# Performance work log

Hardware: AMD Instinct MI355X
Metric: run time of the kernel (lower is better)

The kernel has to match this reference:

```python
import jax, jax.numpy as jnp
import numpy as np

B, Z, OUT, NODES = 2048, 64, 512, 64
TRIPLES = 3 * (NODES - 1)  # (self, left, right) per real node
EPS_BN = 1e-5
EPS_TLN = 1e-5
SLOPE = 0.01  # LeakyReLU default


def setup_inputs() -> dict:
    key = jax.random.key(0)
    ks = jax.random.split(key, 12)
    def n(k, shape, s=0.05):
        return jax.random.normal(k, shape, jnp.float32) * s
    inp = {
        "trees": jax.random.normal(ks[0], (B, Z), jnp.float32),
        "indexes": jax.random.randint(ks[1], (B, TRIPLES, 1), 0, NODES),
        # MLP: Linear(Z,64) -> BN -> Linear(64,256) -> BN -> Linear(256,1024) -> BN -> Linear(1024,4096) -> BN
        "w1": n(ks[2], (64, Z)),      "b1": jnp.zeros((64,), jnp.float32),
        "g1": jnp.ones((64,), jnp.float32),   "be1": jnp.zeros((64,), jnp.float32),
        "w2": n(ks[3], (256, 64)),    "b2": jnp.zeros((256,), jnp.float32),
        "g2": jnp.ones((256,), jnp.float32),  "be2": jnp.zeros((256,), jnp.float32),
        "w3": n(ks[4], (1024, 256)),  "b3": jnp.zeros((1024,), jnp.float32),
        "g3": jnp.ones((1024,), jnp.float32), "be3": jnp.zeros((1024,), jnp.float32),
        "w4": n(ks[5], (4096, 1024)), "b4": jnp.zeros((4096,), jnp.float32),
        "g4": jnp.ones((4096,), jnp.float32), "be4": jnp.zeros((4096,), jnp.float32),
        # BinaryTreeConv weights: Conv1d(in,out,kernel=3,stride=3) -> (out,in,3)
        "cw1": n(ks[6], (128, 64, 3)),  "cb1": jnp.zeros((128,), jnp.float32),
        "cw2": n(ks[7], (256, 128, 3)), "cb2": jnp.zeros((256,), jnp.float32),
        "cw3": n(ks[8], (OUT, 256, 3)), "cb3": jnp.zeros((OUT,), jnp.float32),
    }
    return inp


def _bn(x, g, b):
    # BatchNorm1d in training mode: batch statistics, biased variance
    m = jnp.mean(x, axis=0)
    v = jnp.var(x, axis=0)
    return g * (x - m) * jax.lax.rsqrt(v + EPS_BN) + b


def _lrelu(x):
    return jnp.where(x > 0, x, SLOPE * x)


def _tree_conv(x, idx, w, b):
    # x: (B, C, N); idx: (B, 3M) node indices; w: (O, C, 3)
    Bn, C, _ = x.shape
    expanded = jnp.take_along_axis(x, idx[:, None, :], axis=2)  # (B, C, 3M) gather
    expanded = expanded.reshape(Bn, C, -1, 3)                    # (B, C, M, 3)
    out = jnp.einsum('bcmk,ock->bom', expanded, w) + b[None, :, None]
    zero = jnp.zeros((Bn, w.shape[0], 1), x.dtype)               # re-attach null-node slot
    return jnp.concatenate([zero, out], axis=2)                  # (B, O, M+1)


def _tree_norm(x):
    # TreeLayerNorm: normalize over (channels, nodes) per sample; torch.std is unbiased
    m = jnp.mean(x, axis=(1, 2), keepdims=True)
    s = jnp.std(x, axis=(1, 2), ddof=1, keepdims=True)
    return (x - m) / (s + EPS_TLN)


def reference(trees, indexes, w1, b1, g1, be1, w2, b2, g2, be2, w3, b3, g3, be3,
              w4, b4, g4, be4, cw1, cb1, cw2, cb2, cw3, cb3):
    idx = indexes[..., 0]  # (B, 3M)
    h = _lrelu(_bn(trees @ w1.T + b1, g1, be1))
    h = _lrelu(_bn(h @ w2.T + b2, g2, be2))
    h = _lrelu(_bn(h @ w3.T + b3, g3, be3))
    h = _lrelu(_bn(h @ w4.T + b4, g4, be4))
    x = h.reshape(h.shape[0], 64, 64)  # (B, C=64, N=64)
    x = _lrelu(_tree_norm(_tree_conv(x, idx, cw1, cb1)))
    x = _lrelu(_tree_norm(_tree_conv(x, idx, cw2, cb2)))
    x = _lrelu(_tree_norm(_tree_conv(x, idx, cw3, cb3)))
    return x  # (B, OUT, 64)
```

## Files before the change

kernel.cpp:

```cpp
#include <hip/hip_runtime.h>

typedef unsigned short u16;
typedef unsigned int   u32;
typedef __attribute__((ext_vector_type(8))) short short8;
typedef __attribute__((ext_vector_type(4))) float f32x4;
typedef __attribute__((ext_vector_type(4))) u16  u16x4;

#define DI __device__ __forceinline__

DI float b2f(u16 v){ return __builtin_bit_cast(float, (u32)v << 16); }
DI u16 f2b(float f){ u32 u = __builtin_bit_cast(u32, f); return (u16)((u + 0x7fffu + ((u >> 16) & 1u)) >> 16); }
DI float lrelu(float v){ return v > 0.f ? v : 0.01f * v; }

__global__ __launch_bounds__(256)
void cvt_w_all(const float* __restrict__ w1, u16* __restrict__ d1,
               const float* __restrict__ w2, u16* __restrict__ d2,
               const float* __restrict__ w3, u16* __restrict__ d3,
               const float* __restrict__ w4, u16* __restrict__ d4)
{
  int i = blockIdx.x*256 + threadIdx.x;
  const float* s; u16* d; int li;
  if      (i < 1024)   { s = w1; d = d1; li = i; }
  else if (i < 5120)   { s = w2; d = d2; li = i - 1024; }
  else if (i < 70656)  { s = w3; d = d3; li = i - 5120; }
  else if (i < 1119232){ s = w4; d = d4; li = i - 70656; }
  else return;
  float4 v = ((const float4*)s)[li];
  u16x4 o; o[0]=f2b(v.x); o[1]=f2b(v.y); o[2]=f2b(v.z); o[3]=f2b(v.w);
  *(u16x4*)(d + (size_t)li*4) = o;
}

DI void repack_one(const float* __restrict__ w, u16* __restrict__ wr,
                   int e, int C, int lgC)
{
  int R = 3*C;
  int NK   = R >> 5;
  int j    = e & 7;
  int lane = (e >> 3) & 63;
  int blk  = e >> 9;
  int tr   = blk / NK, kb = blk - tr*NK;
  int row  = tr*16 + (lane & 15);
  int kcol = kb*32 + (lane >> 4)*8 + j;
  int k = kcol >> lgC; int c = kcol & (C-1);
  wr[e] = f2b(w[(size_t)row*R + c*3 + k]);
}

__global__ __launch_bounds__(256)
void repack_all(const float* __restrict__ c1, u16* __restrict__ r1,
                const float* __restrict__ c2, u16* __restrict__ r2,
                const float* __restrict__ c3, u16* __restrict__ r3)
{
  int i = blockIdx.x*256 + threadIdx.x;
  if      (i < 24576)  repack_one(c1, r1, i,          64, 6);
  else if (i < 122880) repack_one(c2, r2, i - 24576, 128, 7);
  else if (i < 516096) repack_one(c3, r3, i - 122880,256, 8);
}

template<int BM, int BN, int WROWS, int WCOLS, int RT, int CT, bool APPLY>
__global__ __launch_bounds__(WROWS*WCOLS*64)
void gemm_bn(const float* __restrict__ A, const u16* __restrict__ W,
             const float* __restrict__ partIn, const float* __restrict__ gA,
             const float* __restrict__ beA, int splitIn,
             float* __restrict__ Y, float* __restrict__ partOut,
             int M, int N, int K)
{
  constexpr int NT  = WROWS*WCOLS*64;
  constexpr int ALD = (BM*4)/NT;
  constexpr int BLD = (BN*4)/NT;
  __shared__ __align__(16) u16 As[BM*32];
  __shared__ __align__(16) u16 Bs[BN*32];
  __shared__ float colS[WROWS][BN], colS2[WROWS][BN];
  __shared__ __align__(16) float ssL[APPLY ? 2048 : 4];
  const int tid  = threadIdx.x;
  const int wave = tid >> 6, lane = tid & 63;
  const int wr = wave / WCOLS, wc = wave % WCOLS;
  const int lrow = lane & 15, kg = lane >> 4;
  const int m0 = blockIdx.x * BM, n0 = blockIdx.y * BN;

  if constexpr (APPLY){
    for (int n = tid; n < K; n += NT){
      float s = 0.f, s2 = 0.f;
      for (int i = 0; i < splitIn; i++){
        s  += partIn[(size_t)(i*2+0)*K + n];
        s2 += partIn[(size_t)(i*2+1)*K + n];
      }
      float inv  = 1.f / (float)M;
      float mean = s * inv;
      float var  = fmaxf(s2*inv - mean*mean, 0.f);
      float sc   = gA[n] * rsqrtf(var + 1e-5f);
      ssL[n]     = sc;
      ssL[K + n] = beA[n] - mean*sc;
    }
    __syncthreads();
  }

  f32x4 acc[RT][CT] = {};
  for (int k0 = 0; k0 < K; k0 += 32) {
    uint4 av[ALD], bv[BLD];
#pragma unroll
    for (int i = 0; i < ALD; i++){
      int x = tid + i*NT; int kc = k0 + (x&3)*8;
      const float* ap = A + (size_t)(m0 + (x>>2))*K + kc;
      float4 y0 = *(const float4*)ap, y1 = *(const float4*)(ap + 4);
      float v[8] = {y0.x,y0.y,y0.z,y0.w,y1.x,y1.y,y1.z,y1.w};
      if constexpr (APPLY){
        float4 c0 = *(const float4*)(ssL + kc),     c1 = *(const float4*)(ssL + kc + 4);
        float4 h0 = *(const float4*)(ssL + K + kc), h1 = *(const float4*)(ssL + K + kc + 4);
        v[0]=lrelu(v[0]*c0.x+h0.x); v[1]=lrelu(v[1]*c0.y+h0.y);
        v[2]=lrelu(v[2]*c0.z+h0.z); v[3]=lrelu(v[3]*c0.w+h0.w);
        v[4]=lrelu(v[4]*c1.x+h1.x); v[5]=lrelu(v[5]*c1.y+h1.y);
        v[6]=lrelu(v[6]*c1.z+h1.z); v[7]=lrelu(v[7]*c1.w+h1.w);
      }
      u32 w0 = (u32)f2b(v[0]) | ((u32)f2b(v[1])<<16);
      u32 w1 = (u32)f2b(v[2]) | ((u32)f2b(v[3])<<16);
      u32 w2 = (u32)f2b(v[4]) | ((u32)f2b(v[5])<<16);
      u32 w3 = (u32)f2b(v[6]) | ((u32)f2b(v[7])<<16);
      av[i] = (uint4){w0,w1,w2,w3};
    }
#pragma unroll
    for (int i = 0; i < BLD; i++){ int x = tid + i*NT; bv[i] = *(const uint4*)(W + (size_t)(n0 + (x>>2))*K + k0 + (x&3)*8); }
    __syncthreads();
#pragma unroll
    for (int i = 0; i < ALD; i++){ *(uint4*)(As + (tid + i*NT)*8) = av[i]; }
#pragma unroll
    for (int i = 0; i < BLD; i++){ *(uint4*)(Bs + (tid + i*NT)*8) = bv[i]; }
    __syncthreads();
    short8 af[RT], bfr[CT];
#pragma unroll
    for (int r = 0; r < RT; r++) af[r]  = *(const short8*)(As + ((wr*RT + r)*16 + lrow)*32 + kg*8);
#pragma unroll
    for (int c = 0; c < CT; c++) bfr[c] = *(const short8*)(Bs + ((wc*CT + c)*16 + lrow)*32 + kg*8);
#pragma unroll
    for (int r = 0; r < RT; r++)
#pragma unroll
      for (int c = 0; c < CT; c++)
        acc[r][c] = __builtin_amdgcn_mfma_f32_16x16x32_bf16(af[r], bfr[c], acc[r][c], 0, 0, 0);
  }
#pragma unroll
  for (int r = 0; r < RT; r++)
#pragma unroll
    for (int c = 0; c < CT; c++)
#pragma unroll
      for (int i = 0; i < 4; i++){
        int m = m0 + (wr*RT + r)*16 + kg*4 + i;
        int n = n0 + (wc*CT + c)*16 + lrow;
        Y[(size_t)m*N + n] = acc[r][c][i];
      }
#pragma unroll
  for (int c = 0; c < CT; c++){
    float s = 0.f, s2 = 0.f;
#pragma unroll
    for (int r = 0; r < RT; r++)
#pragma unroll
      for (int i = 0; i < 4; i++){ float v = acc[r][c][i]; s += v; s2 += v*v; }
    s  += __shfl_xor(s, 16);  s  += __shfl_xor(s, 32);
    s2 += __shfl_xor(s2, 16); s2 += __shfl_xor(s2, 32);
    if (kg == 0){ colS[wr][(wc*CT + c)*16 + lrow] = s; colS2[wr][(wc*CT + c)*16 + lrow] = s2; }
  }
  __syncthreads();
  if (tid < BN){
    float S = 0.f, S2 = 0.f;
#pragma unroll
    for (int w = 0; w < WROWS; w++){ S += colS[w][tid]; S2 += colS2[w][tid]; }
    partOut[(size_t)(blockIdx.x*2+0)*N + n0 + tid] = S;
    partOut[(size_t)(blockIdx.x*2+1)*N + n0 + tid] = S2;
  }
}

__global__ __launch_bounds__(256)
void bn_finalize(const float* __restrict__ part, const float* __restrict__ g,
                 const float* __restrict__ be, float* __restrict__ ss, int N, int M, int split)
{
  int n = blockIdx.x*256 + threadIdx.x;
  if (n >= N) return;
  float s = 0.f, s2 = 0.f;
  for (int i = 0; i < split; i++){ s += part[(size_t)(i*2+0)*N + n]; s2 += part[(size_t)(i*2+1)*N + n]; }
  float inv  = 1.f / (float)M;
  float mean = s * inv;
  float var  = fmaxf(s2*inv - mean*mean, 0.f);
  float sc   = g[n] * rsqrtf(var + 1e-5f);
  ss[n]     = sc;
  ss[N + n] = be[n] - mean*sc;
}

template<int C, int O, int WAVES, int MINW, bool PIPE, bool LAST, bool FIRST>
__global__ __launch_bounds__(WAVES*64, MINW)
void conv_norm(const u16* __restrict__ Xin, const float* __restrict__ XinF,
               const float* __restrict__ ssA,
               const u16* __restrict__ Wr,
               const float* __restrict__ cb, const int* __restrict__ gidx,
               u16* __restrict__ Xout, float* __restrict__ Outf)
{
  constexpr int R    = 3*C;
  constexpr int NK   = R/32;
  constexpr int CSI  = C + 8;
  constexpr int RT   = O/(WAVES*16);
  constexpr int NT   = WAVES*64;
  constexpr int LGC  = (C==64)?6:((C==128)?7:8);
  constexpr int LG32 = LGC - 5;
  __shared__ __align__(16) u16 xs[65*CSI];
  __shared__ int idxs[192];
  __shared__ float red[2*WAVES];
  const int b = blockIdx.x, tid = threadIdx.x;
  const int wave = tid >> 6, lane = tid & 63;
  const int lrow = lane & 15, kg = lane >> 4;

  if constexpr (FIRST){
    const float* yg = XinF + (size_t)b*4096;
    int j0 = tid*8;
    float4 a0 = *(const float4*)(yg + j0);
    float4 a1 = *(const float4*)(yg + j0 + 4);
    float4 s0 = *(const float4*)(ssA + j0);
    float4 s1 = *(const float4*)(ssA + j0 + 4);
    float4 h0 = *(const float4*)(ssA + 4096 + j0);
    float4 h1 = *(const float4*)(ssA + 4096 + j0 + 4);
    int c = j0 >> 6, n0 = j0 & 63;
    u16* xp = xs + c;
    xp[(n0+0)*CSI] = f2b(lrelu(a0.x*s0.x + h0.x));
    xp[(n0+1)*CSI] = f2b(lrelu(a0.y*s0.y + h0.y));
    xp[(n0+2)*CSI] = f2b(lrelu(a0.z*s0.z + h0.z));
    xp[(n0+3)*CSI] = f2b(lrelu(a0.w*s0.w + h0.w));
    xp[(n0+4)*CSI] = f2b(lrelu(a1.x*s1.x + h1.x));
    xp[(n0+5)*CSI] = f2b(lrelu(a1.y*s1.y + h1.y));
    xp[(n0+6)*CSI] = f2b(lrelu(a1.z*s1.z + h1.z));
    xp[(n0+7)*CSI] = f2b(lrelu(a1.w*s1.w + h1.w));
  } else {
    const u16* xg = Xin + (size_t)b*64*C;
    for (int e = tid; e < 64*(C/8); e += NT){
      int row = e/(C/8), t = e%(C/8);
      *(uint4*)(xs + row*CSI + t*8) = *(const uint4*)(xg + row*C + t*8);
    }
  }
  for (int e = tid; e < C/8; e += NT){ uint4 z = {0,0,0,0}; *(uint4*)(xs + 64*CSI + e*8) = z; }
  if (tid < 189){ int v = gidx[b*189 + tid]; idxs[tid] = v & 63; }
  __syncthreads();

  int jr0[4], jr1[4], jr2[4];
#pragma unroll
  for (int ct = 0; ct < 4; ct++){
    int n = ct*16 + lrow;
    jr0[ct] = (n == 0) ? 64 : idxs[3*(n-1) + 0];
    jr1[ct] = (n == 0) ? 64 : idxs[3*(n-1) + 1];
    jr2[ct] = (n == 0) ? 64 : idxs[3*(n-1) + 2];
  }

  const u16* wbase = Wr + ((size_t)wave*NK << 9) + lane*8;

  auto loadA = [&](short8* af, int kb32){
#pragma unroll
    for (int r = 0; r < RT; r++)
      af[r] = *(const short8*)(wbase + (((size_t)(WAVES*r)*NK + kb32) << 9));
  };
  auto loadB = [&](short8* bfr, int kb32){
    const int k  = kb32 >> LG32;
    const int c0 = ((kb32*32) & (C-1)) + kg*8;
#pragma unroll
    for (int ct = 0; ct < 4; ct++){
      int row = (k == 0) ? jr0[ct] : ((k == 1) ? jr1[ct] : jr2[ct]);
      bfr[ct] = *(const short8*)(xs + row*CSI + c0);
    }
  };

  f32x4 acc[RT][4] = {};
  auto domfma = [&](short8* af, short8* bfr){
    __builtin_amdgcn_s_setprio(1);
#pragma unroll
    for (int r = 0; r < RT; r++)
#pragma unroll
      for (int ct = 0; ct < 4; ct++)
        acc[r][ct] = __builtin_amdgcn_mfma_f32_16x16x32_bf16(af[r], bfr[ct], acc[r][ct], 0, 0, 0);
    __builtin_amdgcn_s_setprio(0);
  };

  if constexpr (PIPE) {
    short8 afA[RT], bfA[4], afB[RT], bfB[4];
    loadA(afA, 0); loadB(bfA, 0);
    for (int kb32 = 0; kb32 < NK; kb32 += 2){
      loadA(afB, kb32+1); loadB(bfB, kb32+1);
      domfma(afA, bfA);
      if (kb32 + 2 < NK){ loadA(afA, kb32+2); loadB(bfA, kb32+2); }
      domfma(afB, bfB);
    }
  } else {
    for (int kb32 = 0; kb32 < NK; kb32++){
      short8 af[RT], bfr[4];
      loadA(af, kb32); loadB(bfr, kb32);
      domfma(af, bfr);
    }
  }

  float s = 0.f, s2 = 0.f;
#pragma unroll
  for (int r = 0; r < RT; r++)
#pragma unroll
    for (int i = 0; i < 4; i++){
      int o = (wave + WAVES*r)*16 + kg*4 + i;
      float bias = cb[o];
#pragma unroll
      for (int ct = 0; ct < 4; ct++){
        int n = ct*16 + lrow;
        float v = acc[r][ct][i];
        if (n != 0) v += bias;
        acc[r][ct][i] = v;
        s += v; s2 += v*v;
      }
    }
#pragma unroll
  for (int off = 32; off > 0; off >>= 1){ s += __shfl_down(s, off); s2 += __shfl_down(s2, off); }
  if (lane == 0){ red[wave] = s; red[WAVES + wave] = s2; }
  __syncthreads();
  if (tid == 0){
    float S = 0.f, S2 = 0.f;
    for (int w = 0; w < WAVES; w++){ S += red[w]; S2 += red[WAVES + w]; }
    const float NV = (float)(O*64);
    float mean = S / NV;
    float var  = fmaxf(S2/NV - mean*mean, 0.f) * (NV/(NV-1.f));
    float sc   = 1.f / (sqrtf(var) + 1e-5f);
    red[0] = mean; red[1] = sc;
  }
  __syncthreads();
  const float mean = red[0], sc = red[1];

  if constexpr (LAST) {
#pragma unroll
    for (int r = 0; r < RT; r++)
#pragma unroll
      for (int ct = 0; ct < 4; ct++)
#pragma unroll
        for (int i = 0; i < 4; i++){
          int o = (wave + WAVES*r)*16 + kg*4 + i;
          int n = ct*16 + lrow;
          Outf[(size_t)b*(O*64) + o*64 + n] = lrelu((acc[r][ct][i] - mean)*sc);
        }
  } else {
#pragma unroll
    for (int r = 0; r < RT; r++)
#pragma unroll
      for (int ct = 0; ct < 4; ct++){
        int o0 = (wave + WAVES*r)*16 + kg*4;
        int n  = ct*16 + lrow;
        u16x4 pk;
#pragma unroll
        for (int i = 0; i < 4; i++) pk[i] = f2b(lrelu((acc[r][ct][i] - mean)*sc));
        *(u16x4*)(Xout + (size_t)b*64*O + (size_t)n*O + o0) = pk;
      }
  }
}

extern "C" void kernel_launch(void* const* d_in, const int* in_sizes, int n_in,
                              void* d_out, int out_size, void* d_ws, size_t ws_size,
                              hipStream_t stream)
{
  const float* trees = (const float*)d_in[0];
  const int*   gidx  = (const int*)d_in[1];
  const float* w1 = (const float*)d_in[2];
  const float* g1 = (const float*)d_in[4];  const float* be1 = (const float*)d_in[5];
  const float* w2 = (const float*)d_in[6];
  const float* g2 = (const float*)d_in[8];  const float* be2 = (const float*)d_in[9];
  const float* w3 = (const float*)d_in[10];
  const float* g3 = (const float*)d_in[12]; const float* be3 = (const float*)d_in[13];
  const float* w4 = (const float*)d_in[14];
  const float* g4 = (const float*)d_in[16]; const float* be4 = (const float*)d_in[17];
  const float* cw1 = (const float*)d_in[18]; const float* cb1 = (const float*)d_in[19];
  const float* cw2 = (const float*)d_in[20]; const float* cb2 = (const float*)d_in[21];
  const float* cw3 = (const float*)d_in[22]; const float* cb3 = (const float*)d_in[23];

  char* ws = (char*)d_ws;
  size_t off = 0;
  auto alloc = [&](size_t bytes)->char*{ char* p = ws + off; off += (bytes + 255) & ~(size_t)255; return p; };
  u16*   Wr1   = (u16*)  alloc(128*192*2);
  u16*   Wr2   = (u16*)  alloc(256*384*2);
  u16*   Wr3   = (u16*)  alloc(512*768*2);
  float* partA = (float*)alloc(64*4096*4);
  float* partB = (float*)alloc(64*4096*4);
  float* ss4   = (float*)alloc(2*4096*4);
  u16*   Xc3   = (u16*)  alloc((size_t)2048*64*256*2);

  u16*   ob   = (u16*)d_out;
  float* outF = (float*)d_out;
  float* Ya   = (float*)ob;
  u16*   Wb1  = ob + 19660800;
  u16*   Wb2  = ob + 19664896;
  u16*   Wb3  = ob + 19681280;
  u16*   Wb4  = ob + 19943424;
  u16*   Xc2  = ob + 33554432;
  float* Yb   = (float*)(ob + 50331648);

  cvt_w_all <<<4372, 256, 0, stream>>>(w1, Wb1, w2, Wb2, w3, Wb3, w4, Wb4);
  repack_all<<<2016, 256, 0, stream>>>(cw1, Wr1, cw2, Wr2, cw3, Wr3);

  gemm_bn<64,64,4,1,1,4,false><<<dim3(32,1),  256, 0, stream>>>(trees, Wb1, nullptr, nullptr, nullptr, 0,  Ya, partA, 2048, 64,   64);
  gemm_bn<64,64,4,1,1,4,true ><<<dim3(32,4),  256, 0, stream>>>(Ya,    Wb2, partA,   g1,      be1,     32, Yb, partB, 2048, 256,  64);
  gemm_bn<64,64,4,1,1,4,true ><<<dim3(32,16), 256, 0, stream>>>(Yb,    Wb3, partB,   g2,      be2,     32, Ya, partA, 2048, 1024, 256);
  gemm_bn<128,128,2,2,4,4,true><<<dim3(16,32),256, 0, stream>>>(Ya,    Wb4, partA,   g3,      be3,     32, Yb, partB, 2048, 4096, 1024);
  bn_finalize<<<16, 256, 0, stream>>>(partB, g4, be4, ss4, 4096, 2048, 16);

  conv_norm< 64,128,8,4,true ,false,true ><<<2048, 512, 0, stream>>>(nullptr, Yb, ss4, Wr1, cb1, gidx, Xc2, nullptr);
  conv_norm<128,256,8,4,true ,false,false><<<2048, 512, 0, stream>>>(Xc2, nullptr, nullptr, Wr2, cb2, gidx, Xc3, nullptr);
  conv_norm<256,512,8,4,false,true ,false><<<2048, 512, 0, stream>>>(Xc3, nullptr, nullptr, Wr3, cb3, gidx, nullptr, outF);
}
```

Measured before the change: 350.0 us.

## Split conv waves over output and node tiles, half-split A loads in last layer

The tree-conv kernel used to give every wave all 64 node columns and a slice of output channels. It now uses a 2D wave grid (OG output groups × NG node groups), so each wave loads more weight rows and fewer gathered activation tiles. This changes the balance between global weight reads and LDS gather reads per MFMA. The non-pipelined last layer also loads A fragments in two halves, interleaving loads with MFMAs to lower register pressure.

```diff
diff --git a/kernel.cpp b/kernel.cpp
--- a/kernel.cpp
+++ b/kernel.cpp
@@ -183,8 +183,8 @@
   ss[N + n] = be[n] - mean*sc;
 }
 
-template<int C, int O, int WAVES, int MINW, bool PIPE, bool LAST, bool FIRST>
-__global__ __launch_bounds__(WAVES*64, MINW)
+template<int C, int O, int OG, int NG, int MINW, bool PIPE, bool LAST, bool FIRST>
+__global__ __launch_bounds__(OG*NG*64, MINW)
 void conv_norm(const u16* __restrict__ Xin, const float* __restrict__ XinF,
                const float* __restrict__ ssA,
                const u16* __restrict__ Wr,
@@ -194,8 +194,10 @@
   constexpr int R    = 3*C;
   constexpr int NK   = R/32;
   constexpr int CSI  = C + 8;
-  constexpr int RT   = O/(WAVES*16);
+  constexpr int WAVES= OG*NG;
   constexpr int NT   = WAVES*64;
+  constexpr int RT   = O/(OG*16);
+  constexpr int CTW  = 4/NG;
   constexpr int LGC  = (C==64)?6:((C==128)?7:8);
   constexpr int LG32 = LGC - 5;
   __shared__ __align__(16) u16 xs[65*CSI];
@@ -203,6 +205,7 @@
   __shared__ float red[2*WAVES];
   const int b = blockIdx.x, tid = threadIdx.x;
   const int wave = tid >> 6, lane = tid & 63;
+  const int og = wave / NG, ng = wave % NG;
   const int lrow = lane & 15, kg = lane >> 4;
 
   if constexpr (FIRST){
@@ -235,45 +238,50 @@
   if (tid < 189){ int v = gidx[b*189 + tid]; idxs[tid] = v & 63; }
   __syncthreads();
 
-  int jr0[4], jr1[4], jr2[4];
-#pragma unroll
-  for (int ct = 0; ct < 4; ct++){
-    int n = ct*16 + lrow;
+  int jr0[CTW], jr1[CTW], jr2[CTW];
+#pragma unroll
+  for (int ct = 0; ct < CTW; ct++){
+    int n = (ng*CTW + ct)*16 + lrow;
     jr0[ct] = (n == 0) ? 64 : idxs[3*(n-1) + 0];
     jr1[ct] = (n == 0) ? 64 : idxs[3*(n-1) + 1];
     jr2[ct] = (n == 0) ? 64 : idxs[3*(n-1) + 2];
   }
 
-  const u16* wbase = Wr + ((size_t)wave*NK << 9) + lane*8;
+  const u16* wbase = Wr + ((size_t)og*NK << 9) + lane*8;
 
   auto loadA = [&](short8* af, int kb32){
 #pragma unroll
     for (int r = 0; r < RT; r++)
-      af[r] = *(const short8*)(wbase + (((size_t)(WAVES*r)*NK + kb32) << 9));
+      af[r] = *(const short8*)(wbase + (((size_t)(OG*r)*NK + kb32) << 9));
+  };
+  auto loadAh = [&](short8* af, int kb32, int h){
+#pragma unroll
+    for (int j = 0; j < RT/2; j++)
+      af[j] = *(const short8*)(wbase + (((size_t)(OG*(h*(RT/2) + j))*NK + kb32) << 9));
   };
   auto loadB = [&](short8* bfr, int kb32){
     const int k  = kb32 >> LG32;
     const int c0 = ((kb32*32) & (C-1)) + kg*8;
 #pragma unroll
-    for (int ct = 0; ct < 4; ct++){
+    for (int ct = 0; ct < CTW; ct++){
       int row = (k == 0) ? jr0[ct] : ((k == 1) ? jr1[ct] : jr2[ct]);
       bfr[ct] = *(const short8*)(xs + row*CSI + c0);
     }
   };
 
-  f32x4 acc[RT][4] = {};
-  auto domfma = [&](short8* af, short8* bfr){
-    __builtin_amdgcn_s_setprio(1);
-#pragma unroll
-    for (int r = 0; r < RT; r++)
-#pragma unroll
-      for (int ct = 0; ct < 4; ct++)
-        acc[r][ct] = __builtin_amdgcn_mfma_f32_16x16x32_bf16(af[r], bfr[ct], acc[r][ct], 0, 0, 0);
-    __builtin_amdgcn_s_setprio(0);
-  };
+  f32x4 acc[RT][CTW] = {};
 
   if constexpr (PIPE) {
-    short8 afA[RT], bfA[4], afB[RT], bfB[4];
+    short8 afA[RT], bfA[CTW], afB[RT], bfB[CTW];
+    auto domfma = [&](short8* af, short8* bfr){
+      __builtin_amdgcn_s_setprio(1);
+#pragma unroll
+      for (int r = 0; r < RT; r++)
+#pragma unroll
+        for (int ct = 0; ct < CTW; ct++)
+          acc[r][ct] = __builtin_amdgcn_mfma_f32_16x16x32_bf16(af[r], bfr[ct], acc[r][ct], 0, 0, 0);
+      __builtin_amdgcn_s_setprio(0);
+    };
     loadA(afA, 0); loadB(bfA, 0);
     for (int kb32 = 0; kb32 < NK; kb32 += 2){
       loadA(afB, kb32+1); loadB(bfB, kb32+1);
@@ -283,9 +291,26 @@
     }
   } else {
     for (int kb32 = 0; kb32 < NK; kb32++){
-      short8 af[RT], bfr[4];
-      loadA(af, kb32); loadB(bfr, kb32);
-      domfma(af, bfr);
+      short8 bfr[CTW];
+      loadB(bfr, kb32);
+      short8 af0[RT/2];
+      loadAh(af0, kb32, 0);
+      __builtin_amdgcn_s_setprio(1);
+#pragma unroll
+      for (int j = 0; j < RT/2; j++)
+#pragma unroll
+        for (int ct = 0; ct < CTW; ct++)
+          acc[j][ct] = __builtin_amdgcn_mfma_f32_16x16x32_bf16(af0[j], bfr[ct], acc[j][ct], 0, 0, 0);
+      __builtin_amdgcn_s_setprio(0);
+      short8 af1[RT/2];
+      loadAh(af1, kb32, 1);
+      __builtin_amdgcn_s_setprio(1);
+#pragma unroll
+      for (int j = 0; j < RT/2; j++)
+#pragma unroll
+        for (int ct = 0; ct < CTW; ct++)
+          acc[RT/2 + j][ct] = __builtin_amdgcn_mfma_f32_16x16x32_bf16(af1[j], bfr[ct], acc[RT/2 + j][ct], 0, 0, 0);
+      __builtin_amdgcn_s_setprio(0);
     }
   }
 
@@ -294,11 +319,11 @@
   for (int r = 0; r < RT; r++)
 #pragma unroll
     for (int i = 0; i < 4; i++){
-      int o = (wave + WAVES*r)*16 + kg*4 + i;
+      int o = (og + OG*r)*16 + kg*4 + i;
       float bias = cb[o];
 #pragma unroll
-      for (int ct = 0; ct < 4; ct++){
-        int n = ct*16 + lrow;
+      for (int ct = 0; ct < CTW; ct++){
+        int n = (ng*CTW + ct)*16 + lrow;
         float v = acc[r][ct][i];
         if (n != 0) v += bias;
         acc[r][ct][i] = v;
@@ -325,20 +350,20 @@
 #pragma unroll
     for (int r = 0; r < RT; r++)
 #pragma unroll
-      for (int ct = 0; ct < 4; ct++)
+      for (int ct = 0; ct < CTW; ct++)
 #pragma unroll
         for (int i = 0; i < 4; i++){
-          int o = (wave + WAVES*r)*16 + kg*4 + i;
-          int n = ct*16 + lrow;
+          int o = (og + OG*r)*16 + kg*4 + i;
+          int n = (ng*CTW + ct)*16 + lrow;
           Outf[(size_t)b*(O*64) + o*64 + n] = lrelu((acc[r][ct][i] - mean)*sc);
         }
   } else {
 #pragma unroll
     for (int r = 0; r < RT; r++)
 #pragma unroll
-      for (int ct = 0; ct < 4; ct++){
-        int o0 = (wave + WAVES*r)*16 + kg*4;
-        int n  = ct*16 + lrow;
+      for (int ct = 0; ct < CTW; ct++){
+        int o0 = (og + OG*r)*16 + kg*4;
+        int n  = (ng*CTW + ct)*16 + lrow;
         u16x4 pk;
 #pragma unroll
         for (int i = 0; i < 4; i++) pk[i] = f2b(lrelu((acc[r][ct][i] - mean)*sc));
@@ -395,7 +420,7 @@
   gemm_bn<128,128,2,2,4,4,true><<<dim3(16,32),256, 0, stream>>>(Ya,    Wb4, partA,   g3,      be3,     32, Yb, partB, 2048, 4096, 1024);
   bn_finalize<<<16, 256, 0, stream>>>(partB, g4, be4, ss4, 4096, 2048, 16);
 
-  conv_norm< 64,128,8,4,true ,false,true ><<<2048, 512, 0, stream>>>(nullptr, Yb, ss4, Wr1, cb1, gidx, Xc2, nullptr);
-  conv_norm<128,256,8,4,true ,false,false><<<2048, 512, 0, stream>>>(Xc2, nullptr, nullptr, Wr2, cb2, gidx, Xc3, nullptr);
-  conv_norm<256,512,8,4,false,true ,false><<<2048, 512, 0, stream>>>(Xc3, nullptr, nullptr, Wr3, cb3, gidx, nullptr, outF);
-}
+  conv_norm< 64,128,2,4,4,true ,false,true ><<<2048, 512, 0, stream>>>(nullptr, Yb, ss4, Wr1, cb1, gidx, Xc2, nullptr);
+  conv_norm<128,256,4,2,4,true ,false,false><<<2048, 512, 0, stream>>>(Xc2, nullptr, nullptr, Wr2, cb2, gidx, Xc3, nullptr);
+  conv_norm<256,512,4,2,4,false,true ,false><<<2048, 512, 0, stream>>>(Xc3, nullptr, nullptr, Wr3, cb3, gidx, nullptr, outF);
+}
```

Measured after the change: 365.2 us. 4.3% more time.
